# Optimization experiments

Hardware: AMD Instinct MI355X
Metric: run time of the kernel (lower is better)

Reference implementation:

```python
import jax, jax.numpy as jnp
import numpy as np

T, B, IN_DIM = 2048, 8, 512
D_VALUE, D_KEY = 512, 128
CHUNK = 128
EPS = 1e-8


def setup_inputs() -> dict:
    key = jax.random.key(0)
    ks = jax.random.split(key, 9)
    s = 0.02
    return {
        "x": jax.random.normal(ks[0], (T, B, IN_DIM), dtype=jnp.float32),
        "Wv": jax.random.normal(ks[1], (D_VALUE, IN_DIM), dtype=jnp.float32) * s,
        "bv": jnp.zeros((D_VALUE,), dtype=jnp.float32),
        "Wk": jax.random.normal(ks[2], (D_KEY, IN_DIM), dtype=jnp.float32) * s,
        "bk": jnp.zeros((D_KEY,), dtype=jnp.float32),
        "Wq": jax.random.normal(ks[3], (D_KEY, IN_DIM), dtype=jnp.float32) * s,
        "bq": jnp.zeros((D_KEY,), dtype=jnp.float32),
        "Wa": jax.random.normal(ks[4], (D_KEY, IN_DIM), dtype=jnp.float32) * s,
        "ba": jnp.zeros((D_KEY,), dtype=jnp.float32),
    }


def _gla_forward(x, Wv, bv, Wk, bk, Wq, bq, Wa, ba):
    # Projections: x (T,B,in) -> v (T,B,d), k/q/alpha (T,B,n)
    v = jnp.einsum("tbi,di->tbd", x, Wv) + bv
    k = jnp.einsum("tbi,ni->tbn", x, Wk) + bk
    q = jnp.einsum("tbi,ni->tbn", x, Wq) + bq
    alpha = jax.nn.sigmoid(jnp.einsum("tbi,ni->tbn", x, Wa) + ba)

    Tt, Bb, d = v.shape
    n = k.shape[2]
    nch = Tt // CHUNK  # T chosen divisible by CHUNK

    # Reshape time-major tensors into (n_chunks, C, B, dim)
    v_r = v.reshape(nch, CHUNK, Bb, d)
    k_r = k.reshape(nch, CHUNK, Bb, n)
    q_r = q.reshape(nch, CHUNK, Bb, n)
    a_r = alpha.reshape(nch, CHUNK, Bb, n)

    def chunk_step(S_prev, inp):
        v_ch, k_ch, q_ch, a_ch = inp  # (C,B,d), (C,B,n), (C,B,n), (C,B,n)
        outer = jnp.einsum("tbd,tbn->tbdn", v_ch, k_ch)  # (C,B,d,n)
        cp = jnp.cumprod(jnp.maximum(a_ch, EPS), axis=0)  # (C,B,n)
        inv_prefix = 1.0 / (cp + EPS)
        scaled = jnp.cumsum(outer * inv_prefix[:, :, None, :], axis=0)
        # local decayed state plus carried state decayed by prefix product
        S_local = (scaled + S_prev[None, :, :, :]) * cp[:, :, None, :]
        y_ch = jnp.einsum("tbdn,tbn->tbd", S_local, q_ch)  # S @ q
        return S_local[-1], y_ch

    S0 = jnp.zeros((Bb, d, n), dtype=v.dtype)
    _, y = jax.lax.scan(chunk_step, S0, (v_r, k_r, q_r, a_r))
    return y.reshape(Tt, Bb, d)


def reference(x, Wv, bv, Wk, bk, Wq, bq, Wa, ba):
    return _gla_forward(x, Wv, bv, Wk, bk, Wq, bq, Wa, ba)
```

## Files before the change

kernel.cpp:

```cpp
#include <hip/hip_runtime.h>


#define EPSV 1e-8f

typedef __bf16 bf16x8 __attribute__((ext_vector_type(8)));
typedef __bf16 bf16x4 __attribute__((ext_vector_type(4)));
typedef float f32x4 __attribute__((ext_vector_type(4)));

__device__ __forceinline__ void async_copy16(const void* g, void* l) {
  __builtin_amdgcn_global_load_lds(
      (const __attribute__((address_space(1))) void*)g,
      (__attribute__((address_space(3))) void*)l, 16, 0, 0);
}

__global__ __launch_bounds__(256) void conv_bf16(const float* __restrict__ src,
                                                 __bf16* __restrict__ dst) {
  long i = ((long)blockIdx.x * 256 + threadIdx.x) * 8;
  float4 f0 = *(const float4*)(src + i);
  float4 f1 = *(const float4*)(src + i + 4);
  bf16x8 h;
  h[0] = (__bf16)f0.x; h[1] = (__bf16)f0.y; h[2] = (__bf16)f0.z; h[3] = (__bf16)f0.w;
  h[4] = (__bf16)f1.x; h[5] = (__bf16)f1.y; h[6] = (__bf16)f1.z; h[7] = (__bf16)f1.w;
  *(bf16x8*)(dst + i) = h;
}

__global__ __launch_bounds__(256) void conv_w(const float* __restrict__ Wv,
                                              const float* __restrict__ Wk,
                                              const float* __restrict__ Wq,
                                              const float* __restrict__ Wa,
                                              __bf16* __restrict__ dst) {
  long i = ((long)blockIdx.x * 256 + threadIdx.x) * 8;
  int row = (int)(i >> 9);
  int col = (int)(i & 511);
  const float* src;
  if (row < 512)      src = Wv + (long)row * 512 + col;
  else if (row < 640) src = Wk + (long)(row - 512) * 512 + col;
  else if (row < 768) src = Wq + (long)(row - 640) * 512 + col;
  else                src = Wa + (long)(row - 768) * 512 + col;
  float4 f0 = *(const float4*)(src);
  float4 f1 = *(const float4*)(src + 4);
  bf16x8 h;
  h[0] = (__bf16)f0.x; h[1] = (__bf16)f0.y; h[2] = (__bf16)f0.z; h[3] = (__bf16)f0.w;
  h[4] = (__bf16)f1.x; h[5] = (__bf16)f1.y; h[6] = (__bf16)f1.z; h[7] = (__bf16)f1.w;
  *(bf16x8*)(dst + i) = h;
}

__global__ __launch_bounds__(256) void proj_mfma(
    const __bf16* __restrict__ xb, const __bf16* __restrict__ wcat,
    const float* __restrict__ bv, const float* __restrict__ bk,
    const float* __restrict__ bq, const float* __restrict__ ba,
    __bf16* __restrict__ vt, __bf16* __restrict__ kout,
    __bf16* __restrict__ qout, float* __restrict__ aout) {
  __shared__ __attribute__((aligned(16))) char smem[128 * 136 * 2];
  __bf16* a_sm = (__bf16*)smem;
  __bf16* b_sm = a_sm + 128 * 32;
  __bf16* tr   = (__bf16*)smem;

  int tid = threadIdx.x;
  int lane = tid & 63, wave = tid >> 6;
  int mt = blockIdx.x, nt = blockIdx.y;
  int wr = wave >> 1, wcol = wave & 1;

  const __bf16* xtile = xb + (long)mt * 128 * 512;
  const __bf16* wtile = wcat + (long)nt * 128 * 512;

  f32x4 acc[4][4] = {};
  int lr = lane >> 2, lc = lane & 3;
  int l15 = lane & 15, qd = lane >> 4;
  int slsrc = (lc ^ ((lr >> 1) & 3)) * 8;
  int frd = (l15 >> 1) & 3;

  for (int k0 = 0; k0 < 512; k0 += 32) {
#pragma unroll
    for (int h = 0; h < 2; ++h) {
      int q = wave * 2 + h;
      int row = q * 16 + lr;
      async_copy16(xtile + (long)row * 512 + k0 + slsrc, &a_sm[q * 512]);
      async_copy16(wtile + (long)row * 512 + k0 + slsrc, &b_sm[q * 512]);
    }
    __syncthreads();
    bf16x8 af[4], bfr[4];
#pragma unroll
    for (int t = 0; t < 4; ++t) {
      af[t]  = *(const bf16x8*)&a_sm[(wr * 64 + t * 16 + l15) * 32 + (qd ^ frd) * 8];
      bfr[t] = *(const bf16x8*)&b_sm[(wcol * 64 + t * 16 + l15) * 32 + (qd ^ frd) * 8];
    }
#pragma unroll
    for (int i = 0; i < 4; ++i)
#pragma unroll
      for (int j = 0; j < 4; ++j)
        acc[i][j] = __builtin_amdgcn_mfma_f32_16x16x32_bf16(af[i], bfr[j], acc[i][j], 0, 0, 0);
    __syncthreads();
  }

  if (nt < 4) {
    const float* bias = bv + nt * 128;
#pragma unroll
    for (int i = 0; i < 4; ++i)
#pragma unroll
      for (int j = 0; j < 4; ++j) {
        int col = wcol * 64 + j * 16 + l15;
        float bz = bias[col];
#pragma unroll
        for (int r = 0; r < 4; ++r) {
          int row = wr * 64 + i * 16 + qd * 4 + r;
          tr[col * 136 + (row & 7) * 16 + (row >> 3)] = (__bf16)(acc[i][j][r] + bz);
        }
      }
    __syncthreads();
    int cbase = (mt >> 3) * 8;
    int s0 = (mt & 7) * 16;
#pragma unroll
    for (int it = 0; it < 4; ++it) {
      int p = it * 256 + tid;
      int d = p & 127, b = p >> 7;
      bf16x8 u0 = *(const bf16x8*)&tr[d * 136 + b * 16];
      bf16x8 u1 = *(const bf16x8*)&tr[d * 136 + b * 16 + 8];
      __bf16* dst = vt + ((long)(cbase + b) * 512 + nt * 128 + d) * 128 + s0;
      *(bf16x8*)dst = u0;
      *(bf16x8*)(dst + 8) = u1;
    }
    return;
  }

  const float* bias; bool sig = false;
  __bf16* dstb = nullptr; float* dstf = nullptr;
  if (nt == 4)      { bias = bk; dstb = kout; }
  else if (nt == 5) { bias = bq; dstb = qout; }
  else              { bias = ba; dstf = aout; sig = true; }

#pragma unroll
  for (int i = 0; i < 4; ++i)
#pragma unroll
    for (int j = 0; j < 4; ++j) {
      int col = wcol * 64 + j * 16 + l15;
      float bz = bias[col];
#pragma unroll
      for (int r = 0; r < 4; ++r) {
        int row = wr * 64 + i * 16 + qd * 4 + r;
        float z = acc[i][j][r] + bz;
        long addr = ((long)mt * 128 + row) * 128 + col;
        if (sig) dstf[addr] = 1.f / (1.f + __expf(-z));
        else     dstb[addr] = (__bf16)z;
      }
    }
}

__global__ __launch_bounds__(64) void scan_cp(const float* __restrict__ a,
                                              const __bf16* __restrict__ k,
                                              const __bf16* __restrict__ q,
                                              __bf16* __restrict__ kbs,
                                              __bf16* __restrict__ qb,
                                              __bf16* __restrict__ kt,
                                              float* __restrict__ cpend) {
  int idx = blockIdx.x * 64 + threadIdx.x;
  int n = idx & 127;
  int b = (idx >> 7) & 7;
  int c = idx >> 10;
  long base = ((long)c * 1024 + b) * 128 + n;
  float cp = 1.f;
  __bf16 ktbuf[128];
#pragma unroll
  for (int tt = 0; tt < 128; ++tt) {
    long off = base + (long)tt * 1024;
    float av = fmaxf(a[off], EPSV);
    cp *= av;
    float kk = (float)k[off] / (cp + EPSV);
    float qq = (float)q[off] * cp;
    __bf16 kh = (__bf16)kk;
    kbs[off] = kh;
    qb[off] = (__bf16)qq;
    ktbuf[tt] = kh;
  }
  cpend[(c * 8 + b) * 128 + n] = cp;
  __bf16* dst = kt + ((long)((c * 8 + b) * 128 + n)) * 128;
#pragma unroll
  for (int i = 0; i < 16; ++i) {
    bf16x8 h;
#pragma unroll
    for (int j = 0; j < 8; ++j) h[j] = ktbuf[i * 8 + j];
    *(bf16x8*)(dst + i * 8) = h;
  }
}

__global__ __launch_bounds__(256) void gmm(const __bf16* __restrict__ vt,
                                           const __bf16* __restrict__ kt,
                                           const float* __restrict__ cpend,
                                           __bf16* __restrict__ Gt) {
  int tid = threadIdx.x, lane = tid & 63, wave = tid >> 6;
  int wr = wave >> 1, wc = wave & 1;
  int l15 = lane & 15, qd = lane >> 4;
  int cb = blockIdx.x >> 2, dt = blockIdx.x & 3;
  const __bf16* vbase = vt + ((long)cb * 512 + dt * 128) * 128;
  const __bf16* kbase = kt + (long)cb * 16384;
  f32x4 acc[4][4] = {};
#pragma unroll
  for (int kk = 0; kk < 4; ++kk) {
    int k0 = kk * 32;
    bf16x8 af[4], bfr[4];
#pragma unroll
    for (int i = 0; i < 4; ++i)
      af[i] = *(const bf16x8*)(vbase + (long)(wr * 64 + i * 16 + l15) * 128 + k0 + qd * 8);
#pragma unroll
    for (int j = 0; j < 4; ++j)
      bfr[j] = *(const bf16x8*)(kbase + (long)(wc * 64 + j * 16 + l15) * 128 + k0 + qd * 8);
#pragma unroll
    for (int i = 0; i < 4; ++i)
#pragma unroll
      for (int j = 0; j < 4; ++j)
        acc[i][j] = __builtin_amdgcn_mfma_f32_16x16x32_bf16(af[i], bfr[j], acc[i][j], 0, 0, 0);
  }
  float ce[4];
#pragma unroll
  for (int j = 0; j < 4; ++j) ce[j] = cpend[cb * 128 + wc * 64 + j * 16 + l15];
#pragma unroll
  for (int i = 0; i < 4; ++i)
#pragma unroll
    for (int j = 0; j < 4; ++j) {
      int col = wc * 64 + j * 16 + l15;
#pragma unroll
      for (int r = 0; r < 4; ++r) {
        int row = wr * 64 + i * 16 + qd * 4 + r;
        Gt[((long)cb * 512 + dt * 128 + row) * 128 + col] = (__bf16)(acc[i][j][r] * ce[j]);
      }
    }
}

__global__ __launch_bounds__(256) void scan_state(const __bf16* __restrict__ Gt,
                                                  const float* __restrict__ cpend,
                                                  __bf16* __restrict__ St) {
  long e = ((long)blockIdx.x * 256 + threadIdx.x) * 4;
  int n0 = (int)(e & 127);
  int b = (int)(e >> 16);
  float4 S = {0.f, 0.f, 0.f, 0.f};
#pragma unroll
  for (int c = 0; c < 16; ++c) {
    long idx = (long)c * 524288 + e;
    bf16x4 g = *(const bf16x4*)(Gt + idx);
    bf16x4 sv;
    sv[0] = (__bf16)S.x; sv[1] = (__bf16)S.y;
    sv[2] = (__bf16)S.z; sv[3] = (__bf16)S.w;
    *(bf16x4*)(St + idx) = sv;
    const float4 cp = *(const float4*)(cpend + (c * 8 + b) * 128 + n0);
    S.x = (float)g[0] + S.x * cp.x;
    S.y = (float)g[1] + S.y * cp.y;
    S.z = (float)g[2] + S.z * cp.z;
    S.w = (float)g[3] + S.w * cp.w;
  }
}

__global__ __launch_bounds__(256) void ymm(const __bf16* __restrict__ qb,
                                           const __bf16* __restrict__ kbs,
                                           const __bf16* __restrict__ vt,
                                           const __bf16* __restrict__ St,
                                           float* __restrict__ out) {
  __shared__ __bf16 A_lds[128 * 136];
  int tid = threadIdx.x, lane = tid & 63, wave = tid >> 6;
  int wr = wave >> 1, wc = wave & 1;
  int l15 = lane & 15, qd = lane >> 4;
  int cb = blockIdx.x >> 2, dt = blockIdx.x & 3;
  int c = cb >> 3, b = cb & 7;
  const __bf16* qbase = qb + ((long)c * 1024 + b) * 128;
  const __bf16* kbase = kbs + ((long)c * 1024 + b) * 128;

  {
    f32x4 accA[4][4] = {};
#pragma unroll
    for (int kk = 0; kk < 4; ++kk) {
      int k0 = kk * 32;
      bf16x8 af[4], bfr[4];
#pragma unroll
      for (int i = 0; i < 4; ++i)
        af[i] = *(const bf16x8*)(qbase + (long)(wr * 64 + i * 16 + l15) * 1024 + k0 + qd * 8);
#pragma unroll
      for (int j = 0; j < 4; ++j)
        bfr[j] = *(const bf16x8*)(kbase + (long)(wc * 64 + j * 16 + l15) * 1024 + k0 + qd * 8);
#pragma unroll
      for (int i = 0; i < 4; ++i)
#pragma unroll
        for (int j = 0; j < 4; ++j)
          accA[i][j] = __builtin_amdgcn_mfma_f32_16x16x32_bf16(af[i], bfr[j], accA[i][j], 0, 0, 0);
    }
#pragma unroll
    for (int i = 0; i < 4; ++i)
#pragma unroll
      for (int j = 0; j < 4; ++j) {
        int s = wc * 64 + j * 16 + l15;
#pragma unroll
        for (int r = 0; r < 4; ++r) {
          int t = wr * 64 + i * 16 + qd * 4 + r;
          A_lds[t * 136 + s] = (s <= t) ? (__bf16)accA[i][j][r] : (__bf16)0.f;
        }
      }
  }
  __syncthreads();

  f32x4 acc[4][4] = {};
  const __bf16* vbase = vt + ((long)cb * 512 + dt * 128) * 128;
  const __bf16* sbase = St + ((long)cb * 512 + dt * 128) * 128;
#pragma unroll
  for (int kk = 0; kk < 4; ++kk) {
    int k0 = kk * 32;
    bf16x8 af[4], bfr[4];
#pragma unroll
    for (int i = 0; i < 4; ++i)
      af[i] = *(const bf16x8*)(vbase + (long)(wr * 64 + i * 16 + l15) * 128 + k0 + qd * 8);
#pragma unroll
    for (int j = 0; j < 4; ++j)
      bfr[j] = *(const bf16x8*)&A_lds[(wc * 64 + j * 16 + l15) * 136 + k0 + qd * 8];
#pragma unroll
    for (int i = 0; i < 4; ++i)
#pragma unroll
      for (int j = 0; j < 4; ++j)
        acc[i][j] = __builtin_amdgcn_mfma_f32_16x16x32_bf16(af[i], bfr[j], acc[i][j], 0, 0, 0);
  }
#pragma unroll
  for (int kk = 0; kk < 4; ++kk) {
    int k0 = kk * 32;
    bf16x8 af[4], bfr[4];
#pragma unroll
    for (int i = 0; i < 4; ++i)
      af[i] = *(const bf16x8*)(sbase + (long)(wr * 64 + i * 16 + l15) * 128 + k0 + qd * 8);
#pragma unroll
    for (int j = 0; j < 4; ++j)
      bfr[j] = *(const bf16x8*)(qbase + (long)(wc * 64 + j * 16 + l15) * 1024 + k0 + qd * 8);
#pragma unroll
    for (int i = 0; i < 4; ++i)
#pragma unroll
      for (int j = 0; j < 4; ++j)
        acc[i][j] = __builtin_amdgcn_mfma_f32_16x16x32_bf16(af[i], bfr[j], acc[i][j], 0, 0, 0);
  }

#pragma unroll
  for (int i = 0; i < 4; ++i)
#pragma unroll
    for (int j = 0; j < 4; ++j) {
      int colt = wc * 64 + j * 16 + l15;
      long addr = ((long)(c * 128 + colt) * 8 + b) * 512 + dt * 128 + wr * 64 + i * 16 + qd * 4;
      *(float4*)(out + addr) = *(float4*)&acc[i][j];
    }
}

extern "C" void kernel_launch(void* const* d_in, const int* in_sizes, int n_in,
                              void* d_out, int out_size, void* d_ws, size_t ws_size,
                              hipStream_t stream) {
  const float* x  = (const float*)d_in[0];
  const float* Wv = (const float*)d_in[1];
  const float* bv = (const float*)d_in[2];
  const float* Wk = (const float*)d_in[3];
  const float* bk = (const float*)d_in[4];
  const float* Wq = (const float*)d_in[5];
  const float* bq = (const float*)d_in[6];
  const float* Wa = (const float*)d_in[7];
  const float* ba = (const float*)d_in[8];
  float* out = (float*)d_out;
  float* ws = (float*)d_ws;

  float*  a_buf = ws;
  __bf16* qb    = (__bf16*)(ws + 2097152);
  __bf16* kbs   = (__bf16*)(ws + 3145728);
  __bf16* kt    = (__bf16*)(ws + 4194304);
  __bf16* vt    = (__bf16*)(ws + 5242880);
  __bf16* k_raw = (__bf16*)(ws + 9437184);
  __bf16* q_raw = (__bf16*)(ws + 10485760);
  __bf16* xb    = (__bf16*)(ws + 11534336);
  __bf16* Wcat  = (__bf16*)(ws + 15728640);
  __bf16* Gt    = xb;
  __bf16* St    = (__bf16*)(ws + 15958016);
  float*  cpend = ws + 20152320;

  conv_bf16<<<4096, 256, 0, stream>>>(x, xb);
  conv_w<<<224, 256, 0, stream>>>(Wv, Wk, Wq, Wa, Wcat);
  proj_mfma<<<dim3(128, 7), 256, 0, stream>>>(xb, Wcat, bv, bk, bq, ba,
                                              vt, k_raw, q_raw, a_buf);
  scan_cp<<<256, 64, 0, stream>>>(a_buf, k_raw, q_raw, kbs, qb, kt, cpend);
  gmm<<<512, 256, 0, stream>>>(vt, kt, cpend, Gt);
  scan_state<<<512, 256, 0, stream>>>(Gt, cpend, St);
  ymm<<<512, 256, 0, stream>>>(qb, kbs, vt, St, out);
}
```

Measured before the change: 204.6 us.

## Parallelize cumulative-product scan across time segments within each block

The scan_cp kernel previously ran one thread per (chunk, batch, key) column and walked all 128 timesteps serially, giving only 256 blocks of 64 threads. It now splits each chunk into 8 segments of 16 steps, computes per-segment products, combines them through shared memory into prefixes, then rescales k and q per segment. This raises thread-level parallelism and memory-level parallelism eightfold, at the cost of a barrier, shared memory, and reading alpha values into registers. Summing prefixes sequentially is a slightly different floating-point order than a single serial product.

```diff
diff --git a/kernel.cpp b/kernel.cpp
--- a/kernel.cpp
+++ b/kernel.cpp
@@ -146,36 +146,58 @@
     }
 }
 
-__global__ __launch_bounds__(64) void scan_cp(const float* __restrict__ a,
-                                              const __bf16* __restrict__ k,
-                                              const __bf16* __restrict__ q,
-                                              __bf16* __restrict__ kbs,
-                                              __bf16* __restrict__ qb,
-                                              __bf16* __restrict__ kt,
-                                              float* __restrict__ cpend) {
-  int idx = blockIdx.x * 64 + threadIdx.x;
-  int n = idx & 127;
-  int b = (idx >> 7) & 7;
-  int c = idx >> 10;
+__global__ __launch_bounds__(512) void scan_cp(const float* __restrict__ a,
+                                               const __bf16* __restrict__ k,
+                                               const __bf16* __restrict__ q,
+                                               __bf16* __restrict__ kbs,
+                                               __bf16* __restrict__ qb,
+                                               __bf16* __restrict__ kt,
+                                               float* __restrict__ cpend) {
+  __shared__ float segprod[8][64];
+  int tid = threadIdx.x;
+  int nl = tid & 63;
+  int seg = tid >> 6;
+  int bid = blockIdx.x;
+  int nh = bid & 1;
+  int b = (bid >> 1) & 7;
+  int c = bid >> 4;
+  int n = nh * 64 + nl;
   long base = ((long)c * 1024 + b) * 128 + n;
-  float cp = 1.f;
-  __bf16 ktbuf[128];
-#pragma unroll
-  for (int tt = 0; tt < 128; ++tt) {
-    long off = base + (long)tt * 1024;
-    float av = fmaxf(a[off], EPSV);
-    cp *= av;
+  int t0 = seg * 16;
+
+  float av[16];
+  float p = 1.f;
+#pragma unroll
+  for (int i = 0; i < 16; ++i) {
+    float v = fmaxf(a[base + (long)(t0 + i) * 1024], EPSV);
+    av[i] = v;
+    p *= v;
+  }
+  segprod[seg][nl] = p;
+  __syncthreads();
+
+  float prefix = 1.f;
+#pragma unroll
+  for (int s = 0; s < 7; ++s)
+    if (s < seg) prefix *= segprod[s][nl];
+  if (seg == 7) cpend[(c * 8 + b) * 128 + n] = prefix * p;
+
+  float cp = prefix;
+  __bf16 ktbuf[16];
+#pragma unroll
+  for (int i = 0; i < 16; ++i) {
+    long off = base + (long)(t0 + i) * 1024;
+    cp *= av[i];
     float kk = (float)k[off] / (cp + EPSV);
     float qq = (float)q[off] * cp;
     __bf16 kh = (__bf16)kk;
     kbs[off] = kh;
     qb[off] = (__bf16)qq;
-    ktbuf[tt] = kh;
-  }
-  cpend[(c * 8 + b) * 128 + n] = cp;
-  __bf16* dst = kt + ((long)((c * 8 + b) * 128 + n)) * 128;
-#pragma unroll
-  for (int i = 0; i < 16; ++i) {
+    ktbuf[i] = kh;
+  }
+  __bf16* dst = kt + ((long)((c * 8 + b) * 128 + n)) * 128 + t0;
+#pragma unroll
+  for (int i = 0; i < 2; ++i) {
     bf16x8 h;
 #pragma unroll
     for (int j = 0; j < 8; ++j) h[j] = ktbuf[i * 8 + j];
@@ -373,7 +395,7 @@
   conv_w<<<224, 256, 0, stream>>>(Wv, Wk, Wq, Wa, Wcat);
   proj_mfma<<<dim3(128, 7), 256, 0, stream>>>(xb, Wcat, bv, bk, bq, ba,
                                               vt, k_raw, q_raw, a_buf);
-  scan_cp<<<256, 64, 0, stream>>>(a_buf, k_raw, q_raw, kbs, qb, kt, cpend);
+  scan_cp<<<256, 512, 0, stream>>>(a_buf, k_raw, q_raw, kbs, qb, kt, cpend);
   gmm<<<512, 256, 0, stream>>>(vt, kt, cpend, Gt);
   scan_state<<<512, 256, 0, stream>>>(Gt, cpend, St);
   ymm<<<512, 256, 0, stream>>>(qb, kbs, vt, St, out);
```

New measurement: 185.6 us. 1.1x faster.
